# Kernel optimization log

Hardware: AMD Instinct MI355X
Metric: run time of the kernel (lower is better)

## Reference

```python
import jax, jax.numpy as jnp
import numpy as np

N = 50000
E = 600000
IN_C = 128
HID_C = 128
OUT_C = 128


def _glorot(key, shape):
    fan_in, fan_out = shape[0], shape[1]
    lim = np.sqrt(6.0 / (fan_in + fan_out))
    return jax.random.uniform(key, shape, jnp.float32, -lim, lim)


def setup_inputs() -> dict:
    key = jax.random.key(0)
    ks = jax.random.split(key, 10)
    x = jax.random.normal(ks[0], (N, IN_C), jnp.float32)
    edge_index = jax.random.randint(ks[1], (2, E), 0, N, jnp.int64)
    return {
        "x": x,
        "edge_index": edge_index,
        # SAGEConv1: lin_l (aggregated, with bias) and lin_r (root, no bias)
        "W1_l": _glorot(ks[2], (IN_C, HID_C)),
        "b1_l": jnp.zeros((HID_C,), jnp.float32),
        "W1_r": _glorot(ks[3], (IN_C, HID_C)),
        # SAGEConv2
        "W2_l": _glorot(ks[4], (HID_C, OUT_C)),
        "b2_l": jnp.zeros((OUT_C,), jnp.float32),
        "W2_r": _glorot(ks[5], (HID_C, OUT_C)),
        # final Linear(hidden+out -> out)
        "W_lin": _glorot(ks[6], (HID_C + OUT_C, OUT_C)),
        "b_lin": jnp.zeros((OUT_C,), jnp.float32),
    }


def _sage_conv(x, src, dst, W_l, b_l, W_r):
    # mean-aggregate source features onto destination nodes
    msg = x[src]                                   # [E, C] gather
    agg = jax.ops.segment_sum(msg, dst, num_segments=N)        # [N, C]
    cnt = jax.ops.segment_sum(jnp.ones((src.shape[0],), x.dtype), dst,
                              num_segments=N)                   # [N]
    mean = agg / jnp.maximum(cnt, 1.0)[:, None]
    return mean @ W_l + b_l + x @ W_r


def reference(x, edge_index, W1_l, b1_l, W1_r, W2_l, b2_l, W2_r, W_lin, b_lin):
    src, dst = edge_index[0], edge_index[1]
    x1 = jax.nn.relu(_sage_conv(x, src, dst, W1_l, b1_l, W1_r))   # [N, HID]
    x2 = jax.nn.relu(_sage_conv(x1, src, dst, W2_l, b2_l, W2_r))  # [N, OUT]
    return jnp.concatenate([x1, x2], axis=-1) @ W_lin + b_lin     # [N, OUT]
```

## Files before the change

### kernel.cpp

```cpp
#include <hip/hip_runtime.h>


typedef _Float16 f16;
typedef unsigned int u32;
typedef __attribute__((ext_vector_type(4))) _Float16 f16x4;
typedef __attribute__((ext_vector_type(8))) _Float16 f16x8;
typedef __attribute__((ext_vector_type(4))) float f32x4;

#define RNB 128

__global__ void prep_kernel(const float* __restrict__ x, f16* __restrict__ xh, int n4,
                            const int* __restrict__ ei, int* __restrict__ ghist, int E,
                            const float* __restrict__ W1l, const float* __restrict__ W1r,
                            const float* __restrict__ W2l, const float* __restrict__ W2r,
                            const float* __restrict__ Wlin, f16* __restrict__ wt,
                            int cb, int wb) {
  int b = blockIdx.x;
  if (b < cb) {
    int i = b * 256 + threadIdx.x;
    if (i < n4) {
      const float4 v = ((const float4*)x)[i];
      f16x4 h = { (f16)v.x, (f16)v.y, (f16)v.z, (f16)v.w };
      ((f16x4*)xh)[i] = h;
    }
  } else if (b < cb + wb) {
    int tid = (b - cb) * 256 + threadIdx.x;
    int w = tid >> 15, idx = tid & 32767;
    int j = idx & 7, n = (idx >> 3) & 127, chunk = idx >> 10;
    int k = chunk * 8 + j;
    float v;
    if (w == 0) v = (k < 128) ? W1l[k * 128 + n] : W1r[(k - 128) * 128 + n];
    else if (w == 1) v = (k < 128) ? W2l[k * 128 + n] : W2r[(k - 128) * 128 + n];
    else v = Wlin[k * 128 + n];
    wt[tid] = (f16)v;
  } else {
    __shared__ int h[256];
    int tid = threadIdx.x, rb = b - cb - wb;
    h[tid] = 0;
    __syncthreads();
    int per = (E + RNB - 1) / RNB;
    int s = rb * per, e = s + per; if (e > E) e = E;
    for (int i = s + tid; i < e; i += 256) atomicAdd(&h[ei[E + i] >> 8], 1);
    __syncthreads();
    ghist[tid * RNB + rb] = h[tid];
  }
}

__global__ void scan_block_kernel(const int* __restrict__ in, int* __restrict__ out,
                                  int* __restrict__ sums, int n) {
  __shared__ int s[2][1024];
  int t = threadIdx.x;
  int gid = blockIdx.x * 1024 + t;
  int v = (gid < n) ? in[gid] : 0;
  int cur = 0;
  s[0][t] = v;
  __syncthreads();
  for (int ofs = 1; ofs < 1024; ofs <<= 1) {
    int nv = s[cur][t] + ((t >= ofs) ? s[cur][t - ofs] : 0);
    s[cur ^ 1][t] = nv;
    cur ^= 1;
    __syncthreads();
  }
  if (gid < n) out[gid] = s[cur][t] - v;
  if (t == 1023) sums[blockIdx.x] = s[cur][1023];
}

__device__ inline void sums_prefix(const int* sums, int* pf) {
  int t = threadIdx.x;
  if (t < 32) {
    int v = sums[t];
    int incl = v;
#pragma unroll
    for (int ofs = 1; ofs < 32; ofs <<= 1) {
      int u = __shfl_up(incl, ofs);
      if (t >= ofs) incl += u;
    }
    pf[t] = incl - v;
  }
}

__global__ void radix_scatter(const int* __restrict__ ei, const int* __restrict__ sg,
                              const int* __restrict__ sums, u32* __restrict__ tmp, int E) {
  __shared__ int cur[256];
  __shared__ int pf[32];
  int tid = threadIdx.x, b = blockIdx.x;
  sums_prefix(sums, pf);
  __syncthreads();
  cur[tid] = sg[tid * RNB + b] + pf[tid >> 3];
  __syncthreads();
  int per = (E + RNB - 1) / RNB;
  int s = b * per, e = s + per; if (e > E) e = E;
  for (int i = s + tid; i < e; i += 256) {
    int d = ei[E + i], sr = ei[i];
    int pos = atomicAdd(&cur[d >> 8], 1);
    tmp[pos] = ((u32)sr << 8) | (u32)(d & 255);
  }
}

__global__ void radix_bucket(const u32* __restrict__ tmp, const int* __restrict__ sg,
                             const int* __restrict__ sums, int* __restrict__ srcs,
                             int* __restrict__ off, int N, int E, int HB) {
  __shared__ int h[256], sc[256], cur[256];
  __shared__ int pf[32];
  int tid = threadIdx.x, hb = blockIdx.x;
  sums_prefix(sums, pf);
  __syncthreads();
  int start = sg[hb * RNB] + pf[hb >> 3];
  int end = (hb + 1 < HB) ? (sg[(hb + 1) * RNB] + pf[(hb + 1) >> 3]) : E;
  h[tid] = 0;
  __syncthreads();
  for (int i = start + tid; i < end; i += 256) atomicAdd(&h[tmp[i] & 255u], 1);
  __syncthreads();
  sc[tid] = h[tid];
  __syncthreads();
  for (int o = 1; o < 256; o <<= 1) {
    int u = (tid >= o) ? sc[tid - o] : 0;
    __syncthreads();
    sc[tid] += u;
    __syncthreads();
  }
  int excl = sc[tid] - h[tid];
  int v = (hb << 8) + tid;
  if (v < N) off[v] = start + excl;
  if (hb == 0 && tid == 0) off[N] = E;
  cur[tid] = start + excl;
  __syncthreads();
  for (int i = start + tid; i < end; i += 256) {
    u32 p = tmp[i];
    int pos = atomicAdd(&cur[p & 255u], 1);
    srcs[pos] = (int)(p >> 8);
  }
}

#define AGG_R 6
__global__ void aggregate_kernel(const f16* __restrict__ feat, const int* __restrict__ off,
                                 const int* __restrict__ srcs, f16* __restrict__ meanf, int n) {
  int pair = (int)((blockIdx.x * blockDim.x + threadIdx.x) >> 6);
  int w0 = pair * 2;
  if (w0 >= n) return;
  int w1 = w0 + 1;
  int lane = threadIdx.x & 63;
  int sub = lane >> 4, n15 = lane & 15;
  int beg0 = off[w0], end0 = off[w0 + 1];
  int beg1 = end0;
  int end1 = (w1 < n) ? off[w1 + 1] : end0;
  int deg0 = end0 - beg0, deg1 = end1 - beg1;

  int s0[AGG_R], s1[AGG_R];
  bool v0[AGG_R], v1[AGG_R];
#pragma unroll
  for (int k = 0; k < AGG_R; ++k) {
    int p = 4 * k + sub;
    v0[k] = p < deg0;  s0[k] = v0[k] ? srcs[beg0 + p] : 0;
    v1[k] = p < deg1;  s1[k] = v1[k] ? srcs[beg1 + p] : 0;
  }
  f16x8 g0[AGG_R], g1[AGG_R];
#pragma unroll
  for (int k = 0; k < AGG_R; ++k) {
    if (v0[k]) g0[k] = *(const f16x8*)(feat + (size_t)s0[k] * 128 + n15 * 8);
    if (v1[k]) g1[k] = *(const f16x8*)(feat + (size_t)s1[k] * 128 + n15 * 8);
  }
  float acc0[8] = {}, acc1[8] = {};
#pragma unroll
  for (int k = 0; k < AGG_R; ++k) {
    if (v0[k]) {
#pragma unroll
      for (int j = 0; j < 8; ++j) acc0[j] += (float)g0[k][j];
    }
    if (v1[k]) {
#pragma unroll
      for (int j = 0; j < 8; ++j) acc1[j] += (float)g1[k][j];
    }
  }
  for (int e = beg0 + 4 * AGG_R; e < end0; e += 4) {
    if (sub < end0 - e) {
      int s = srcs[e + sub];
      f16x8 g = *(const f16x8*)(feat + (size_t)s * 128 + n15 * 8);
#pragma unroll
      for (int j = 0; j < 8; ++j) acc0[j] += (float)g[j];
    }
  }
  for (int e = beg1 + 4 * AGG_R; e < end1; e += 4) {
    if (sub < end1 - e) {
      int s = srcs[e + sub];
      f16x8 g = *(const f16x8*)(feat + (size_t)s * 128 + n15 * 8);
#pragma unroll
      for (int j = 0; j < 8; ++j) acc1[j] += (float)g[j];
    }
  }
#pragma unroll
  for (int j = 0; j < 8; ++j) {
    acc0[j] += __shfl_xor(acc0[j], 16);
    acc0[j] += __shfl_xor(acc0[j], 32);
    acc1[j] += __shfl_xor(acc1[j], 16);
    acc1[j] += __shfl_xor(acc1[j], 32);
  }
  if (sub == 0) {
    float inv = 1.0f / fmaxf((float)deg0, 1.0f);
    f16x8 o;
#pragma unroll
    for (int j = 0; j < 8; ++j) o[j] = (f16)(acc0[j] * inv);
    *(f16x8*)(meanf + (size_t)w0 * 128 + n15 * 8) = o;
  } else if (sub == 1 && w1 < n) {
    float inv = 1.0f / fmaxf((float)deg1, 1.0f);
    f16x8 o;
#pragma unroll
    for (int j = 0; j < 8; ++j) o[j] = (f16)(acc1[j] * inv);
    *(f16x8*)(meanf + (size_t)w1 * 128 + n15 * 8) = o;
  }
}

template <bool RELU, bool OUT16>
__global__ __launch_bounds__(256, 2) void gemm_kernel(
    const f16* __restrict__ U, const f16* __restrict__ V, const f16* __restrict__ Wt,
    const float* __restrict__ bias, void* __restrict__ outp, int M) {
  __shared__ f16 ldsb[32768];
  int tid = threadIdx.x;
  int wave = tid >> 6, lane = tid & 63;
  int quad = lane >> 4, n15 = lane & 15;
  int m0 = blockIdx.x * 128 + wave * 32;
  int kq = quad * 8;

  f16x8 a[2][8];
#pragma unroll
  for (int r = 0; r < 2; ++r) {
    int row = m0 + r * 16 + n15;
    int rowc = row < M ? row : M - 1;
    const f16* bu = U + (size_t)rowc * 128 + kq;
    const f16* bv = V + (size_t)rowc * 128 + kq;
#pragma unroll
    for (int kk = 0; kk < 4; ++kk) a[r][kk] = *(const f16x8*)(bu + kk * 32);
#pragma unroll
    for (int kk = 4; kk < 8; ++kk) a[r][kk] = *(const f16x8*)(bv + (kk - 4) * 32);
  }

#pragma unroll
  for (int it = 0; it < 16; ++it) {
    int idx = it * 256 + tid;
    ((f16x8*)ldsb)[idx] = ((const f16x8*)Wt)[idx];
  }
  __syncthreads();

  f32x4 acc[2][8] = {};
#pragma unroll
  for (int kk = 0; kk < 8; ++kk) {
#pragma unroll
    for (int t = 0; t < 8; ++t) {
      f16x8 b = ((const f16x8*)ldsb)[(kk * 4 + quad) * 128 + t * 16 + n15];
#pragma unroll
      for (int r = 0; r < 2; ++r)
        acc[r][t] = __builtin_amdgcn_mfma_f32_16x16x32_f16(a[r][kk], b, acc[r][t], 0, 0, 0);
    }
  }

  int rbase0 = m0 + quad * 4;
#pragma unroll
  for (int t = 0; t < 8; ++t) {
    float bv = bias[t * 16 + n15];
#pragma unroll
    for (int r = 0; r < 2; ++r) {
#pragma unroll
      for (int i = 0; i < 4; ++i) {
        int row = rbase0 + r * 16 + i;
        if (row < M) {
          float v = acc[r][t][i] + bv;
          if (RELU) v = fmaxf(v, 0.f);
          size_t idx = (size_t)row * 128 + t * 16 + n15;
          if (OUT16) ((f16*)outp)[idx] = (f16)v;
          else       ((float*)outp)[idx] = v;
        }
      }
    }
  }
}

extern "C" void kernel_launch(void* const* d_in, const int* in_sizes, int n_in,
                              void* d_out, int out_size, void* d_ws, size_t ws_size,
                              hipStream_t stream) {
  (void)n_in; (void)out_size; (void)ws_size;
  const float* x    = (const float*)d_in[0];
  const int*   ei   = (const int*)d_in[1];
  const float* W1l  = (const float*)d_in[2];
  const float* b1l  = (const float*)d_in[3];
  const float* W1r  = (const float*)d_in[4];
  const float* W2l  = (const float*)d_in[5];
  const float* b2l  = (const float*)d_in[6];
  const float* W2r  = (const float*)d_in[7];
  const float* Wlin = (const float*)d_in[8];
  const float* blin = (const float*)d_in[9];
  const int N = in_sizes[0] / 128;
  const int E = in_sizes[1] / 2;

  char* ws = (char*)d_ws;
  size_t o = 0;
  auto alloc = [&](size_t bytes) {
    char* p = ws + o;
    o = (o + bytes + 255) & ~(size_t)255;
    return p;
  };
  f16*  xh   = (f16*)alloc((size_t)N * 128 * 2);
  f16*  x1h  = (f16*)alloc((size_t)N * 128 * 2);
  f16*  x2h  = (f16*)alloc((size_t)N * 128 * 2);
  f16*  mh   = (f16*)alloc((size_t)N * 128 * 2);
  f16*  wt   = (f16*)alloc((size_t)3 * 32768 * 2);
  int*  off  = (int*)alloc(((size_t)N + 1) * 4);
  int*  srcs = (int*)alloc((size_t)E * 4);
  u32*  tmp  = (u32*)alloc((size_t)E * 4);
  int*  ghist= (int*)alloc(256 * RNB * 4);
  int*  sg   = (int*)alloc(256 * RNB * 4);
  int*  sums = (int*)alloc(64 * 4);
  f16* wt1 = wt, *wt2 = wt + 32768, *wt3 = wt + 65536;

  const int n4 = N * 128 / 4;
  const int cb = (n4 + 255) / 256;
  const int wb = (3 * 32768) / 256;
  const int HB = (N + 255) / 256;
  const int SN = 256 * RNB;
  const int snb = SN / 1024;

  prep_kernel<<<cb + wb + RNB, 256, 0, stream>>>(x, xh, n4, ei, ghist, E,
                                                 W1l, W1r, W2l, W2r, Wlin, wt, cb, wb);
  scan_block_kernel<<<snb, 1024, 0, stream>>>(ghist, sg, sums, SN);
  radix_scatter<<<RNB, 256, 0, stream>>>(ei, sg, sums, tmp, E);
  radix_bucket<<<HB, 256, 0, stream>>>(tmp, sg, sums, srcs, off, N, E, HB);

  const int aggBlocks  = ((N + 1) / 2 + 3) / 4;
  const int gemmBlocks = (N + 127) / 128;

  aggregate_kernel<<<aggBlocks, 256, 0, stream>>>(xh, off, srcs, mh, N);
  gemm_kernel<true, true><<<gemmBlocks, 256, 0, stream>>>(mh, xh, wt1, b1l, x1h, N);
  aggregate_kernel<<<aggBlocks, 256, 0, stream>>>(x1h, off, srcs, mh, N);
  gemm_kernel<true, true><<<gemmBlocks, 256, 0, stream>>>(mh, x1h, wt2, b2l, x2h, N);
  gemm_kernel<false, false><<<gemmBlocks, 256, 0, stream>>>(x1h, x2h, wt3, blin, d_out, N);
}
```

Measured before the change: 226.7 us.

## Fuse layer-2 and final GEMMs, drop separate histogram scan kernel

Adds a fused kernel that computes the second SAGE layer GEMM, applies bias and ReLU, stages the x2 tile in swizzled shared memory, and feeds it straight into the final linear GEMM together with the x1 registers already loaded. This avoids writing x2 to global memory, reading it back, and one kernel launch. Separately, the scan kernel is removed: the scatter and bucket kernels now each recompute the prefix sums they need from the raw histogram by summing rows and doing a block-level scan. That removes a launch at the cost of redundant per-block histogram reads.

```diff
diff --git a/kernel.cpp b/kernel.cpp
--- a/kernel.cpp
+++ b/kernel.cpp
@@ -46,47 +46,34 @@
   }
 }
 
-__global__ void scan_block_kernel(const int* __restrict__ in, int* __restrict__ out,
-                                  int* __restrict__ sums, int n) {
-  __shared__ int s[2][1024];
-  int t = threadIdx.x;
-  int gid = blockIdx.x * 1024 + t;
-  int v = (gid < n) ? in[gid] : 0;
-  int cur = 0;
-  s[0][t] = v;
-  __syncthreads();
-  for (int ofs = 1; ofs < 1024; ofs <<= 1) {
-    int nv = s[cur][t] + ((t >= ofs) ? s[cur][t - ofs] : 0);
-    s[cur ^ 1][t] = nv;
-    cur ^= 1;
-    __syncthreads();
-  }
-  if (gid < n) out[gid] = s[cur][t] - v;
-  if (t == 1023) sums[blockIdx.x] = s[cur][1023];
-}
-
-__device__ inline void sums_prefix(const int* sums, int* pf) {
-  int t = threadIdx.x;
-  if (t < 32) {
-    int v = sums[t];
-    int incl = v;
-#pragma unroll
-    for (int ofs = 1; ofs < 32; ofs <<= 1) {
-      int u = __shfl_up(incl, ofs);
-      if (t >= ofs) incl += u;
-    }
-    pf[t] = incl - v;
-  }
-}
-
-__global__ void radix_scatter(const int* __restrict__ ei, const int* __restrict__ sg,
-                              const int* __restrict__ sums, u32* __restrict__ tmp, int E) {
+__device__ inline int block_excl_scan256(int v, int* ws) {
+  int lane = threadIdx.x & 63, w = threadIdx.x >> 6;
+  int incl = v;
+#pragma unroll
+  for (int o = 1; o < 64; o <<= 1) {
+    int u = __shfl_up(incl, o);
+    if (lane >= o) incl += u;
+  }
+  if (lane == 63) ws[w] = incl;
+  __syncthreads();
+  int base = 0;
+#pragma unroll
+  for (int i = 0; i < 4; ++i) base += (i < w) ? ws[i] : 0;
+  return base + incl - v;
+}
+
+__global__ void radix_scatter(const int* __restrict__ ei, const int* __restrict__ ghist,
+                              u32* __restrict__ tmp, int E) {
   __shared__ int cur[256];
-  __shared__ int pf[32];
+  __shared__ int ws[4];
   int tid = threadIdx.x, b = blockIdx.x;
-  sums_prefix(sums, pf);
-  __syncthreads();
-  cur[tid] = sg[tid * RNB + b] + pf[tid >> 3];
+  const int* row = ghist + tid * RNB;
+  int part = 0, rest = 0;
+  for (int i = 0; i < b; ++i) part += row[i];
+  for (int i = b; i < RNB; ++i) rest += row[i];
+  int total = part + rest;
+  int excl = block_excl_scan256(total, ws);
+  cur[tid] = excl + part;
   __syncthreads();
   int per = (E + RNB - 1) / RNB;
   int s = b * per, e = s + per; if (e > E) e = E;
@@ -97,18 +84,24 @@
   }
 }
 
-__global__ void radix_bucket(const u32* __restrict__ tmp, const int* __restrict__ sg,
-                             const int* __restrict__ sums, int* __restrict__ srcs,
-                             int* __restrict__ off, int N, int E, int HB) {
+__global__ void radix_bucket(const u32* __restrict__ tmp, const int* __restrict__ ghist,
+                             int* __restrict__ srcs, int* __restrict__ off,
+                             int N, int E, int HB) {
   __shared__ int h[256], sc[256], cur[256];
-  __shared__ int pf[32];
+  __shared__ int bsc[257];
+  __shared__ int ws[4];
   int tid = threadIdx.x, hb = blockIdx.x;
-  sums_prefix(sums, pf);
-  __syncthreads();
-  int start = sg[hb * RNB] + pf[hb >> 3];
-  int end = (hb + 1 < HB) ? (sg[(hb + 1) * RNB] + pf[(hb + 1) >> 3]) : E;
+  const int* row = ghist + tid * RNB;
+  int total = 0;
+#pragma unroll 4
+  for (int i = 0; i < RNB; ++i) total += row[i];
+  int excl = block_excl_scan256(total, ws);
+  bsc[tid] = excl;
+  if (tid == 255) bsc[256] = E;
   h[tid] = 0;
   __syncthreads();
+  int start = bsc[hb];
+  int end = bsc[hb + 1];
   for (int i = start + tid; i < end; i += 256) atomicAdd(&h[tmp[i] & 255u], 1);
   __syncthreads();
   sc[tid] = h[tid];
@@ -119,11 +112,11 @@
     sc[tid] += u;
     __syncthreads();
   }
-  int excl = sc[tid] - h[tid];
+  int exclb = sc[tid] - h[tid];
   int v = (hb << 8) + tid;
-  if (v < N) off[v] = start + excl;
+  if (v < N) off[v] = start + exclb;
   if (hb == 0 && tid == 0) off[N] = E;
-  cur[tid] = start + excl;
+  cur[tid] = start + exclb;
   __syncthreads();
   for (int i = start + tid; i < end; i += 256) {
     u32 p = tmp[i];
@@ -269,6 +262,111 @@
           if (OUT16) ((f16*)outp)[idx] = (f16)v;
           else       ((float*)outp)[idx] = v;
         }
+      }
+    }
+  }
+}
+
+__global__ __launch_bounds__(256, 2) void gemm23_kernel(
+    const f16* __restrict__ U,
+    const f16* __restrict__ V,
+    const f16* __restrict__ Wt2, const f16* __restrict__ Wt3,
+    const float* __restrict__ b2, const float* __restrict__ b3,
+    float* __restrict__ out, int M) {
+  __shared__ f16 ldsb[32768];
+  int tid = threadIdx.x;
+  int wave = tid >> 6, lane = tid & 63;
+  int quad = lane >> 4, n15 = lane & 15;
+  int m0 = blockIdx.x * 128 + wave * 32;
+  int kq = quad * 8;
+
+  f16x8 a[2][8];
+#pragma unroll
+  for (int r = 0; r < 2; ++r) {
+    int row = m0 + r * 16 + n15;
+    int rowc = row < M ? row : M - 1;
+    const f16* bu = U + (size_t)rowc * 128 + kq;
+    const f16* bv = V + (size_t)rowc * 128 + kq;
+#pragma unroll
+    for (int kk = 0; kk < 4; ++kk) a[r][kk] = *(const f16x8*)(bu + kk * 32);
+#pragma unroll
+    for (int kk = 4; kk < 8; ++kk) a[r][kk] = *(const f16x8*)(bv + (kk - 4) * 32);
+  }
+
+#pragma unroll
+  for (int it = 0; it < 16; ++it) {
+    int idx = it * 256 + tid;
+    ((f16x8*)ldsb)[idx] = ((const f16x8*)Wt2)[idx];
+  }
+  __syncthreads();
+
+  f32x4 acc[2][8] = {};
+#pragma unroll
+  for (int kk = 0; kk < 8; ++kk) {
+#pragma unroll
+    for (int t = 0; t < 8; ++t) {
+      f16x8 b = ((const f16x8*)ldsb)[(kk * 4 + quad) * 128 + t * 16 + n15];
+#pragma unroll
+      for (int r = 0; r < 2; ++r)
+        acc[r][t] = __builtin_amdgcn_mfma_f32_16x16x32_f16(a[r][kk], b, acc[r][t], 0, 0, 0);
+    }
+  }
+
+  __syncthreads();
+
+#pragma unroll
+  for (int t = 0; t < 8; ++t) {
+    float bv = b2[t * 16 + n15];
+    int chunk = t * 2 + (n15 >> 3);
+    int offc = n15 & 7;
+#pragma unroll
+    for (int r = 0; r < 2; ++r) {
+#pragma unroll
+      for (int i = 0; i < 4; ++i) {
+        int rowl = wave * 32 + r * 16 + quad * 4 + i;
+        float v = fmaxf(acc[r][t][i] + bv, 0.f);
+        ldsb[rowl * 128 + (((chunk ^ (rowl & 15)) << 3) | offc)] = (f16)v;
+      }
+    }
+  }
+  __syncthreads();
+
+  f16x8 a2[2][4];
+#pragma unroll
+  for (int r = 0; r < 2; ++r) {
+    int rowl = wave * 32 + r * 16 + n15;
+#pragma unroll
+    for (int kk2 = 0; kk2 < 4; ++kk2) {
+      int chunk = kk2 * 4 + quad;
+      a2[r][kk2] = *(const f16x8*)(ldsb + rowl * 128 + ((chunk ^ (rowl & 15)) << 3));
+    }
+  }
+
+  f32x4 acc3[2][8] = {};
+#pragma unroll
+  for (int kk = 0; kk < 8; ++kk) {
+#pragma unroll
+    for (int t = 0; t < 8; ++t) {
+      f16x8 b = ((const f16x8*)Wt3)[(kk * 4 + quad) * 128 + t * 16 + n15];
+#pragma unroll
+      for (int r = 0; r < 2; ++r) {
+        f16x8 av = (kk < 4) ? a[r][4 + kk] : a2[r][kk - 4];
+        acc3[r][t] = __builtin_amdgcn_mfma_f32_16x16x32_f16(av, b, acc3[r][t], 0, 0, 0);
+      }
+    }
+  }
+
+  int rbase0 = m0 + quad * 4;
+#pragma unroll
+  for (int t = 0; t < 8; ++t) {
+    float bv = b3[t * 16 + n15];
+#pragma unroll
+    for (int r = 0; r < 2; ++r) {
+#pragma unroll
+      for (int i = 0; i < 4; ++i) {
+        int row = rbase0 + r * 16 + i;
+        if (row < M)
+          out[(size_t)row * 128 + t * 16 + n15] = acc3[r][t][i] + bv;
       }
     }
   }
@@ -300,29 +398,23 @@
   };
   f16*  xh   = (f16*)alloc((size_t)N * 128 * 2);
   f16*  x1h  = (f16*)alloc((size_t)N * 128 * 2);
-  f16*  x2h  = (f16*)alloc((size_t)N * 128 * 2);
   f16*  mh   = (f16*)alloc((size_t)N * 128 * 2);
   f16*  wt   = (f16*)alloc((size_t)3 * 32768 * 2);
   int*  off  = (int*)alloc(((size_t)N + 1) * 4);
   int*  srcs = (int*)alloc((size_t)E * 4);
   u32*  tmp  = (u32*)alloc((size_t)E * 4);
   int*  ghist= (int*)alloc(256 * RNB * 4);
-  int*  sg   = (int*)alloc(256 * RNB * 4);
-  int*  sums = (int*)alloc(64 * 4);
   f16* wt1 = wt, *wt2 = wt + 32768, *wt3 = wt + 65536;
 
   const int n4 = N * 128 / 4;
   const int cb = (n4 + 255) / 256;
   const int wb = (3 * 32768) / 256;
   const int HB = (N + 255) / 256;
-  const int SN = 256 * RNB;
-  const int snb = SN / 1024;
 
   prep_kernel<<<cb + wb + RNB, 256, 0, stream>>>(x, xh, n4, ei, ghist, E,
                                                  W1l, W1r, W2l, W2r, Wlin, wt, cb, wb);
-  scan_block_kernel<<<snb, 1024, 0, stream>>>(ghist, sg, sums, SN);
-  radix_scatter<<<RNB, 256, 0, stream>>>(ei, sg, sums, tmp, E);
-  radix_bucket<<<HB, 256, 0, stream>>>(tmp, sg, sums, srcs, off, N, E, HB);
+  radix_scatter<<<RNB, 256, 0, stream>>>(ei, ghist, tmp, E);
+  radix_bucket<<<HB, 256, 0, stream>>>(tmp, ghist, srcs, off, N, E, HB);
 
   const int aggBlocks  = ((N + 1) / 2 + 3) / 4;
   const int gemmBlocks = (N + 127) / 128;
@@ -330,6 +422,6 @@
   aggregate_kernel<<<aggBlocks, 256, 0, stream>>>(xh, off, srcs, mh, N);
   gemm_kernel<true, true><<<gemmBlocks, 256, 0, stream>>>(mh, xh, wt1, b1l, x1h, N);
   aggregate_kernel<<<aggBlocks, 256, 0, stream>>>(x1h, off, srcs, mh, N);
-  gemm_kernel<true, true><<<gemmBlocks, 256, 0, stream>>>(mh, x1h, wt2, b2l, x2h, N);
-  gemm_kernel<false, false><<<gemmBlocks, 256, 0, stream>>>(x1h, x2h, wt3, blin, d_out, N);
-}
+  gemm23_kernel<<<gemmBlocks, 256, 0, stream>>>(mh, x1h, wt2, wt3, b2l, blin,
+                                                (float*)d_out, N);
+}
```

Measured after the change: 229.0 us. About the same (+1.0%).
